# Optimization experiments

Measured on AMD Instinct MI355X. Metric: run time of the kernel, lower is better.

## Reference

```python
import jax, jax.numpy as jnp
import numpy as np

V = 100000
E = 1250000
C_IN = 64
C_OUT = 64


def setup_inputs() -> dict:
    key = jax.random.key(0)
    ks = jax.random.split(key, 6)
    X = jax.random.normal(ks[0], (V, C_IN), dtype=jnp.float32)
    edge_src = jax.random.randint(ks[1], (E,), 0, V, dtype=jnp.int32)
    edge_dst = jax.random.randint(ks[2], (E,), 0, V, dtype=jnp.int32)
    edge_w = jax.random.uniform(ks[3], (E,), dtype=jnp.float32)
    # xavier_normal for (C_IN, C_OUT) weight
    std = float(np.sqrt(2.0 / (C_IN + C_OUT)))
    W = jax.random.normal(ks[4], (C_IN, C_OUT), dtype=jnp.float32) * std
    b = jax.random.normal(ks[5], (C_OUT,), dtype=jnp.float32) * 0.0  # bias init zeros
    return {"X": X, "edge_src": edge_src, "edge_dst": edge_dst,
            "edge_w": edge_w, "W": W, "b": b}


def reference(X, edge_src, edge_dst, edge_w, W, b):
    # f = A @ X  (sparse COO spmm): f[dst] += w * X[src]
    msgs = edge_w[:, None] * X[edge_src]                 # [E, C_IN]
    f = jax.ops.segment_sum(msgs, edge_dst, num_segments=X.shape[0])  # [V, C_IN]
    # out = f @ W + b
    return f @ W + b
```

## Files before the change

### kernel.cpp

```cpp
#include <hip/hip_runtime.h>
#include <hip/hip_fp16.h>


constexpr int V = 100000;
constexpr int E = 1250000;
constexpr int C = 64;

constexpr int NBKT = 1024;
constexpr int VB   = 98;
constexpr int BCAP = 1536;
constexpr int FL   = 12;
constexpr int OVF_CAP = 16384;

constexpr size_t Y_OFF    = 0;
constexpr size_t BIN_OFF  = 12800000;
constexpr size_t GCNT_OFF = 25382912;
constexpr size_t OC_OFF   = 25387008;
constexpr size_t OVF_OFF  = 25387024;
constexpr size_t WS_NEW   = 25649168;

using bf16x8 = __attribute__((ext_vector_type(8))) short;
using f32x4  = __attribute__((ext_vector_type(4))) float;

__device__ __forceinline__ short f2bf(float x) {
    unsigned u = __float_as_uint(x);
    unsigned r = u + 0x7fffu + ((u >> 16) & 1u);
    return (short)(r >> 16);
}
__device__ __forceinline__ float bf2f(short h) {
    return __uint_as_float(((unsigned)(unsigned short)h) << 16);
}

constexpr int ZB  = 1;
constexpr int NBM = 1563;

__global__ __launch_bounds__(256) void zero_xw_kernel(const float* __restrict__ X,
                                                      const float* __restrict__ W,
                                                      __half* __restrict__ Y,
                                                      int* __restrict__ gcnt,
                                                      int* __restrict__ oc) {
    if (blockIdx.x < ZB) {
        int i = threadIdx.x;
        #pragma unroll
        for (int j = 0; j < NBKT / 256; ++j) gcnt[i + j * 256] = 0;
        if (i == 0) *oc = 0;
        return;
    }
    __shared__ short Whi[64 * 72];
    __shared__ short Wlo[64 * 72];
    for (int idx = threadIdx.x; idx < 4096; idx += 256) {
        int k = idx >> 6, c = idx & 63;
        float w  = W[idx];
        short hi = f2bf(w);
        short lo = f2bf(w - bf2f(hi));
        Whi[c * 72 + k] = hi;
        Wlo[c * 72 + k] = lo;
    }
    __syncthreads();

    const int wave = threadIdx.x >> 6;
    const int lane = threadIdx.x & 63;
    const int m = lane & 15;
    const int q = lane >> 4;

    bf16x8 bhi[4][2], blo[4][2];
    #pragma unroll
    for (int t = 0; t < 4; ++t)
        #pragma unroll
        for (int h = 0; h < 2; ++h) {
            int o = (t * 16 + m) * 72 + h * 32 + q * 8;
            bhi[t][h] = *(const bf16x8*)&Whi[o];
            blo[t][h] = *(const bf16x8*)&Wlo[o];
        }

    const int chunk = (blockIdx.x - ZB) * 4 + wave;
    if (chunk >= V / 16) return;
    {
        const float* xp = X + (chunk * 16 + m) * 64 + q * 8;
        bf16x8 ahi[2], alo[2];
        #pragma unroll
        for (int h = 0; h < 2; ++h) {
            float4 f0 = *(const float4*)(xp + h * 32);
            float4 f1 = *(const float4*)(xp + h * 32 + 4);
            float f[8] = {f0.x, f0.y, f0.z, f0.w, f1.x, f1.y, f1.z, f1.w};
            #pragma unroll
            for (int j = 0; j < 8; ++j) {
                short hi = f2bf(f[j]);
                ahi[h][j] = hi;
                alo[h][j] = f2bf(f[j] - bf2f(hi));
            }
        }
        #pragma unroll
        for (int t = 0; t < 4; ++t) {
            f32x4 acc = {0.f, 0.f, 0.f, 0.f};
            #pragma unroll
            for (int h = 0; h < 2; ++h) {
                acc = __builtin_amdgcn_mfma_f32_16x16x32_bf16(ahi[h], bhi[t][h], acc, 0, 0, 0);
                acc = __builtin_amdgcn_mfma_f32_16x16x32_bf16(alo[h], bhi[t][h], acc, 0, 0, 0);
                acc = __builtin_amdgcn_mfma_f32_16x16x32_bf16(ahi[h], blo[t][h], acc, 0, 0, 0);
            }
            #pragma unroll
            for (int i = 0; i < 4; ++i) {
                int row = chunk * 16 + q * 4 + i;
                Y[row * 64 + t * 16 + m] = __float2half(acc[i]);
            }
        }
    }
}

constexpr int BIN_BLOCKS = 256;
constexpr int BIN_T      = 1024;

__global__ __launch_bounds__(BIN_T) void bin_kernel(const int*   __restrict__ esrc,
                                                    const int*   __restrict__ edst,
                                                    const float* __restrict__ ew,
                                                    int*  __restrict__ gcnt,
                                                    int2* __restrict__ binned,
                                                    int*  __restrict__ oc,
                                                    int4* __restrict__ ovf) {
    __shared__ int2 stage[NBKT][FL];
    __shared__ int  lcnt[NBKT];
    for (int i = threadIdx.x; i < NBKT; i += BIN_T) lcnt[i] = 0;
    __syncthreads();

    const int iters = (E + BIN_BLOCKS * BIN_T - 1) / (BIN_BLOCKS * BIN_T);
    for (int it = 0; it < iters; ++it) {
        int e = (it * BIN_BLOCKS + blockIdx.x) * BIN_T + threadIdx.x;
        if (e < E) {
            int d = edst[e];
            int s = esrc[e];
            float w = ew[e];
            int bkt = d / VB;
            int ld  = d - bkt * VB;
            int2 rec = make_int2((ld << 17) | s, __float_as_int(w));
            int pos = atomicAdd(&lcnt[bkt], 1);
            if (pos < FL) {
                stage[bkt][pos] = rec;
            } else {
                int g = atomicAdd(&gcnt[bkt], 1);
                if (g < BCAP) binned[bkt * BCAP + g] = rec;
                else { int p = atomicAdd(oc, 1);
                       if (p < OVF_CAP) ovf[p] = make_int4(s, d, __float_as_int(w), 0); }
            }
        }
    }
    __syncthreads();
    for (int b = threadIdx.x; b < NBKT; b += BIN_T) {
        int n = lcnt[b]; n = n < FL ? n : FL;
        if (n > 0) {
            int g = atomicAdd(&gcnt[b], n);
            for (int i = 0; i < n; ++i) {
                int gi = g + i;
                int2 r = stage[b][i];
                if (gi < BCAP) binned[b * BCAP + gi] = r;
                else { int s = r.x & 0x1FFFF; int ld = r.x >> 17;
                       int p = atomicAdd(oc, 1);
                       if (p < OVF_CAP) ovf[p] = make_int4(s, b * VB + ld, r.y, 0); }
            }
        }
    }
}

__global__ __launch_bounds__(512) void bucket_gather_kernel(const int*  __restrict__ gcnt,
                                                            const int2* __restrict__ binned,
                                                            const __half* __restrict__ Y,
                                                            const float* __restrict__ bias,
                                                            float* __restrict__ out) {
    __shared__ int2 raw[BCAP];
    __shared__ int2 sorted[BCAP];
    __shared__ int  cnt[VB];
    __shared__ int  pre[VB];
    __shared__ int  cur[VB];
    __shared__ int  buf[128];

    const int tid = threadIdx.x;
    const int b   = blockIdx.x;
    int n = gcnt[b]; n = n < BCAP ? n : BCAP;

    for (int i = tid; i < VB; i += 512) cnt[i] = 0;
    __syncthreads();

    const int2* src = binned + b * BCAP;
    for (int i = tid; i < n; i += 512) {
        int2 r = src[i];
        raw[i] = r;
        atomicAdd(&cnt[r.x >> 17], 1);
    }
    __syncthreads();

    int x = 0;
    if (tid < 128) { x = (tid < VB) ? cnt[tid] : 0; buf[tid] = x; }
    __syncthreads();
    #pragma unroll
    for (int ofs = 1; ofs < 128; ofs <<= 1) {
        int t = 0;
        if (tid < 128 && tid >= ofs) t = buf[tid - ofs];
        __syncthreads();
        if (tid < 128) buf[tid] += t;
        __syncthreads();
    }
    if (tid < VB) { int ex = buf[tid] - x; pre[tid] = ex; cur[tid] = ex; }
    __syncthreads();

    for (int i = tid; i < n; i += 512) {
        int2 r = raw[i];
        int ld = r.x >> 17;
        int p = atomicAdd(&cur[ld], 1);
        sorted[p] = r;
    }
    __syncthreads();

    const int lane = tid & 63;
    const int wv   = tid >> 6;
    float bias_l = bias[lane];

    for (int ld = wv; ld < VB; ld += 8) {
        int v = b * VB + ld;
        if (v >= V) break;
        int beg = pre[ld];
        int end = beg + cnt[ld];
        float acc = 0.f;
        int i = beg;
        for (; i + 4 <= end; i += 4) {
            int2 r0 = sorted[i], r1 = sorted[i + 1], r2 = sorted[i + 2], r3 = sorted[i + 3];
            float y0 = __half2float(Y[(r0.x & 0x1FFFF) * C + lane]);
            float y1 = __half2float(Y[(r1.x & 0x1FFFF) * C + lane]);
            float y2 = __half2float(Y[(r2.x & 0x1FFFF) * C + lane]);
            float y3 = __half2float(Y[(r3.x & 0x1FFFF) * C + lane]);
            acc += __int_as_float(r0.y) * y0;
            acc += __int_as_float(r1.y) * y1;
            acc += __int_as_float(r2.y) * y2;
            acc += __int_as_float(r3.y) * y3;
        }
        for (; i < end; ++i) {
            int2 rr = sorted[i];
            acc += __int_as_float(rr.y) * __half2float(Y[(rr.x & 0x1FFFF) * C + lane]);
        }
        out[v * C + lane] = acc + bias_l;
    }
}

__global__ __launch_bounds__(256) void ovf_kernel(const int* __restrict__ oc,
                                                  const int4* __restrict__ ovf,
                                                  const __half* __restrict__ Y,
                                                  float* __restrict__ out) {
    int n = *oc;
    n = n < OVF_CAP ? n : OVF_CAP;
    const int lane = threadIdx.x & 63;
    const int nw = gridDim.x * 4;
    for (int e = blockIdx.x * 4 + (threadIdx.x >> 6); e < n; e += nw) {
        int4 rr = ovf[e];
        atomicAdd(&out[rr.y * C + lane],
                  __int_as_float(rr.z) * __half2float(Y[rr.x * C + lane]));
    }
}

__global__ __launch_bounds__(256) void xw_kernel(const float* __restrict__ X,
                                                 const float* __restrict__ W,
                                                 float* __restrict__ Y) {
    __shared__ float Ws[64][64];
    const float4* W4 = (const float4*)W;
    float4* Ws4 = (float4*)&Ws[0][0];
    #pragma unroll
    for (int i = 0; i < 4; ++i)
        Ws4[threadIdx.x + 256 * i] = W4[threadIdx.x + 256 * i];
    __syncthreads();
    const int wave = threadIdx.x >> 6;
    const int lane = threadIdx.x & 63;
    for (int row = blockIdx.x * 4 + wave; row < V; row += gridDim.x * 4) {
        float xv = X[row * C + lane];
        float acc = 0.f;
        #pragma unroll
        for (int k = 0; k < C; ++k)
            acc += __shfl(xv, k, 64) * Ws[k][lane];
        Y[row * C + lane] = acc;
    }
}

__global__ __launch_bounds__(256) void init_out_kernel(const float* __restrict__ b,
                                                       float4* __restrict__ out4) {
    int tid = blockIdx.x * 256 + threadIdx.x;
    const int n4 = V * (C / 4);
    if (tid < n4) {
        const float4* b4 = (const float4*)b;
        out4[tid] = b4[tid & 15];
    }
}

__global__ __launch_bounds__(256) void scatter_kernel(const int*   __restrict__ esrc,
                                                      const int*   __restrict__ edst,
                                                      const float* __restrict__ ew,
                                                      const float* __restrict__ Y,
                                                      float*       __restrict__ out) {
    unsigned tid = blockIdx.x * 256u + threadIdx.x;
    unsigned e = tid >> 4;
    if (e >= (unsigned)E) return;
    int g = (tid & 15) * 4;
    int   s  = esrc[e];
    int   d  = edst[e];
    float we = ew[e];
    float4 y = *(const float4*)(Y + s * C + g);
    float* o = out + (size_t)d * C + g;
    atomicAdd(o + 0, we * y.x);
    atomicAdd(o + 1, we * y.y);
    atomicAdd(o + 2, we * y.z);
    atomicAdd(o + 3, we * y.w);
}

extern "C" void kernel_launch(void* const* d_in, const int* in_sizes, int n_in,
                              void* d_out, int out_size, void* d_ws, size_t ws_size,
                              hipStream_t stream) {
    const float* X    = (const float*)d_in[0];
    const int*   esrc = (const int*)  d_in[1];
    const int*   edst = (const int*)  d_in[2];
    const float* ew   = (const float*)d_in[3];
    const float* W    = (const float*)d_in[4];
    const float* b    = (const float*)d_in[5];
    float* out = (float*)d_out;

    char* ws = (char*)d_ws;

    if (ws_size >= WS_NEW) {
        __half* Y     = (__half*)(ws + Y_OFF);
        int2*  binned = (int2*)(ws + BIN_OFF);
        int*   gcnt   = (int*) (ws + GCNT_OFF);
        int*   oc     = (int*) (ws + OC_OFF);
        int4*  ovf    = (int4*)(ws + OVF_OFF);

        zero_xw_kernel<<<ZB + NBM, 256, 0, stream>>>(X, W, Y, gcnt, oc);
        bin_kernel<<<BIN_BLOCKS, BIN_T, 0, stream>>>(esrc, edst, ew, gcnt, binned, oc, ovf);
        bucket_gather_kernel<<<NBKT, 512, 0, stream>>>(gcnt, binned, Y, b, out);
        ovf_kernel<<<64, 256, 0, stream>>>(oc, ovf, Y, out);
    } else {
        float* Y = (float*)(ws + Y_OFF);
        xw_kernel<<<1024, 256, 0, stream>>>(X, W, Y);
        init_out_kernel<<<(V * (C / 4) + 255) / 256, 256, 0, stream>>>(b, (float4*)out);
        scatter_kernel<<<(E * 16 + 255) / 256, 256, 0, stream>>>(esrc, edst, ew, Y, out);
    }
}
```

Before: 144.1 us.

## Fold overflow handling into bucket gather and deepen gather unroll

Removes the separate overflow kernel launch. Each output vertex now linearly scans the overflow list inside the bucket gather kernel and adds any matching edges before storing. The gather loop also gets an 8-way unrolled stage so more Y loads are in flight, and the per-bucket local staging depth in binning shrinks from 12 to 8. The risk is that every vertex scans the whole overflow list, so cost grows with overflow count; normally the list is small or empty.

Result: no change. 145.1 us (+0.7%).

```diff
diff --git a/kernel.cpp b/kernel.cpp
--- a/kernel.cpp
+++ b/kernel.cpp
@@ -9,7 +9,7 @@
 constexpr int NBKT = 1024;
 constexpr int VB   = 98;
 constexpr int BCAP = 1536;
-constexpr int FL   = 12;
+constexpr int FL   = 8;
 constexpr int OVF_CAP = 16384;
 
 constexpr size_t Y_OFF    = 0;
@@ -163,6 +163,8 @@
 
 __global__ __launch_bounds__(512) void bucket_gather_kernel(const int*  __restrict__ gcnt,
                                                             const int2* __restrict__ binned,
+                                                            const int*  __restrict__ oc,
+                                                            const int4* __restrict__ ovf,
                                                             const __half* __restrict__ Y,
                                                             const float* __restrict__ bias,
                                                             float* __restrict__ out) {
@@ -213,6 +215,7 @@
     const int lane = tid & 63;
     const int wv   = tid >> 6;
     float bias_l = bias[lane];
+    int ovn = *oc; ovn = ovn < OVF_CAP ? ovn : OVF_CAP;
 
     for (int ld = wv; ld < VB; ld += 8) {
         int v = b * VB + ld;
@@ -221,6 +224,28 @@
         int end = beg + cnt[ld];
         float acc = 0.f;
         int i = beg;
+        for (; i + 8 <= end; i += 8) {
+            int2 r0 = sorted[i],     r1 = sorted[i + 1];
+            int2 r2 = sorted[i + 2], r3 = sorted[i + 3];
+            int2 r4 = sorted[i + 4], r5 = sorted[i + 5];
+            int2 r6 = sorted[i + 6], r7 = sorted[i + 7];
+            float y0 = __half2float(Y[(r0.x & 0x1FFFF) * C + lane]);
+            float y1 = __half2float(Y[(r1.x & 0x1FFFF) * C + lane]);
+            float y2 = __half2float(Y[(r2.x & 0x1FFFF) * C + lane]);
+            float y3 = __half2float(Y[(r3.x & 0x1FFFF) * C + lane]);
+            float y4 = __half2float(Y[(r4.x & 0x1FFFF) * C + lane]);
+            float y5 = __half2float(Y[(r5.x & 0x1FFFF) * C + lane]);
+            float y6 = __half2float(Y[(r6.x & 0x1FFFF) * C + lane]);
+            float y7 = __half2float(Y[(r7.x & 0x1FFFF) * C + lane]);
+            acc += __int_as_float(r0.y) * y0;
+            acc += __int_as_float(r1.y) * y1;
+            acc += __int_as_float(r2.y) * y2;
+            acc += __int_as_float(r3.y) * y3;
+            acc += __int_as_float(r4.y) * y4;
+            acc += __int_as_float(r5.y) * y5;
+            acc += __int_as_float(r6.y) * y6;
+            acc += __int_as_float(r7.y) * y7;
+        }
         for (; i + 4 <= end; i += 4) {
             int2 r0 = sorted[i], r1 = sorted[i + 1], r2 = sorted[i + 2], r3 = sorted[i + 3];
             float y0 = __half2float(Y[(r0.x & 0x1FFFF) * C + lane]);
@@ -236,22 +261,12 @@
             int2 rr = sorted[i];
             acc += __int_as_float(rr.y) * __half2float(Y[(rr.x & 0x1FFFF) * C + lane]);
         }
+        for (int k = 0; k < ovn; ++k) {
+            int4 rr = ovf[k];
+            if (rr.y == v)
+                acc += __int_as_float(rr.z) * __half2float(Y[rr.x * C + lane]);
+        }
         out[v * C + lane] = acc + bias_l;
-    }
-}
-
-__global__ __launch_bounds__(256) void ovf_kernel(const int* __restrict__ oc,
-                                                  const int4* __restrict__ ovf,
-                                                  const __half* __restrict__ Y,
-                                                  float* __restrict__ out) {
-    int n = *oc;
-    n = n < OVF_CAP ? n : OVF_CAP;
-    const int lane = threadIdx.x & 63;
-    const int nw = gridDim.x * 4;
-    for (int e = blockIdx.x * 4 + (threadIdx.x >> 6); e < n; e += nw) {
-        int4 rr = ovf[e];
-        atomicAdd(&out[rr.y * C + lane],
-                  __int_as_float(rr.z) * __half2float(Y[rr.x * C + lane]));
     }
 }
 
@@ -329,8 +344,7 @@
 
         zero_xw_kernel<<<ZB + NBM, 256, 0, stream>>>(X, W, Y, gcnt, oc);
         bin_kernel<<<BIN_BLOCKS, BIN_T, 0, stream>>>(esrc, edst, ew, gcnt, binned, oc, ovf);
-        bucket_gather_kernel<<<NBKT, 512, 0, stream>>>(gcnt, binned, Y, b, out);
-        ovf_kernel<<<64, 256, 0, stream>>>(oc, ovf, Y, out);
+        bucket_gather_kernel<<<NBKT, 512, 0, stream>>>(gcnt, binned, oc, ovf, Y, b, out);
     } else {
         float* Y = (float*)(ws + Y_OFF);
         xw_kernel<<<1024, 256, 0, stream>>>(X, W, Y);
```
